# Performance work log

Hardware: AMD Instinct MI355X
Metric: run time of the kernel (lower is better)

Reference implementation:

```python
import jax, jax.numpy as jnp
import numpy as np

N = 50000
E = 1_600_000
IN_C = 128
HID = 64
HEADS = 2
OUT_C = 16
NEG_SLOPE = 0.2
EPS = 1e-16


def setup_inputs() -> dict:
    key = jax.random.key(0)
    ks = jax.random.split(key, 10)
    x = jax.random.normal(ks[0], (N, IN_C), dtype=jnp.float32)
    edge_index = jax.random.randint(ks[1], (2, E), 0, N, dtype=jnp.int64)
    # layer 1: in -> HEADS * HID, concat=True
    s1 = 1.0 / np.sqrt(IN_C)
    W1 = jax.random.normal(ks[2], (IN_C, HEADS * HID), dtype=jnp.float32) * s1
    att_src1 = jax.random.normal(ks[3], (HEADS, HID), dtype=jnp.float32) * (1.0 / np.sqrt(HID))
    att_dst1 = jax.random.normal(ks[4], (HEADS, HID), dtype=jnp.float32) * (1.0 / np.sqrt(HID))
    b1 = jnp.zeros((HEADS * HID,), dtype=jnp.float32)
    # layer 2: HEADS*HID -> OUT_C, heads=1
    s2 = 1.0 / np.sqrt(HEADS * HID)
    W2 = jax.random.normal(ks[5], (HEADS * HID, OUT_C), dtype=jnp.float32) * s2
    att_src2 = jax.random.normal(ks[6], (1, OUT_C), dtype=jnp.float32) * (1.0 / np.sqrt(OUT_C))
    att_dst2 = jax.random.normal(ks[7], (1, OUT_C), dtype=jnp.float32) * (1.0 / np.sqrt(OUT_C))
    b2 = jnp.zeros((OUT_C,), dtype=jnp.float32)
    return {"x": x, "W1": W1, "att_src1": att_src1, "att_dst1": att_dst1, "b1": b1,
            "W2": W2, "att_src2": att_src2, "att_dst2": att_dst2, "b2": b2,
            "edge_index": edge_index}


def gat_conv(x, edge_index, W, att_src, att_dst, bias, heads, out_ch):
    """PyG-style GATConv: per-head linear, additive attention, softmax over
    incoming edges of each destination node, scatter-add aggregation."""
    n = x.shape[0]
    src, dst = edge_index[0], edge_index[1]
    h = (x @ W).reshape(n, heads, out_ch)                # [N,H,C]
    a_src = jnp.einsum('nhc,hc->nh', h, att_src)          # [N,H]
    a_dst = jnp.einsum('nhc,hc->nh', h, att_dst)          # [N,H]
    e = a_src[src] + a_dst[dst]                           # [E,H]
    e = jnp.where(e >= 0, e, NEG_SLOPE * e)               # LeakyReLU(0.2)
    e_max = jax.ops.segment_max(e, dst, num_segments=n)   # [N,H]
    e_max = jax.lax.stop_gradient(jnp.where(jnp.isfinite(e_max), e_max, 0.0))
    e_exp = jnp.exp(e - e_max[dst])                       # [E,H]
    denom = jax.ops.segment_sum(e_exp, dst, num_segments=n)  # [N,H]
    alpha = e_exp / (denom[dst] + EPS)                    # [E,H]
    msg = h[src] * alpha[:, :, None]                      # [E,H,C] (dominant traffic)
    out = jax.ops.segment_sum(msg, dst, num_segments=n)   # [N,H,C]
    return out.reshape(n, heads * out_ch) + bias


def reference(x, W1, att_src1, att_dst1, b1, W2, att_src2, att_dst2, b2, edge_index):
    h = gat_conv(x, edge_index, W1, att_src1, att_dst1, b1, HEADS, HID)
    h = jax.nn.elu(h)
    h = gat_conv(h, edge_index, W2, att_src2, att_dst2, b2, 1, OUT_C)
    return jax.nn.softmax(h, axis=1)
```

## Files before the change

kernel.cpp:

```cpp
#include <hip/hip_runtime.h>
#include <hip/hip_fp16.h>
#include <cstdint>
#include <cstddef>

#define N_NODES 50000
#define N_EDGES 1600000
#define NEG_SLOPE 0.2f
#define GAT_EPS 1e-16f

#define NCHUNK 128
#define CE (N_EDGES / NCHUNK)
#define NBKT 196
#define GEMM_BLOCKS 782

typedef _Float16 half8v __attribute__((ext_vector_type(8)));
typedef _Float16 half4v __attribute__((ext_vector_type(4)));
typedef float f32x4 __attribute__((ext_vector_type(4)));



__global__ __launch_bounds__(256) void k_gh(
    const float* __restrict__ x, const float* __restrict__ W1,
    const float* __restrict__ W2, const float* __restrict__ b1,
    const float* __restrict__ att_src, const float* __restrict__ att_dst,
    _Float16* __restrict__ h1p, float* __restrict__ a_src, float* __restrict__ a_dst,
    const int* __restrict__ ei, int* __restrict__ coarse,
    float* __restrict__ w2tp, float* __restrict__ b1p) {
    __shared__ __align__(16) char smem[34816];
    int t = threadIdx.x;
    int b = blockIdx.x;
    if (b == GEMM_BLOCKS + NCHUNK) {
        for (int i = t; i < 2112; i += 256) {
            int j = i / 132, kp = i % 132;
            float v = 0.f;
            if (kp < 128) {
                int real = (kp & 7) * 16 + (kp >> 3);
                v = W2[real * 16 + j];
            }
            w2tp[i] = v;
        }
        if (t < 128) {
            int real = (t & 7) * 16 + (t >> 3);
            b1p[t] = b1[real];
        }
        return;
    }
    if (b >= GEMM_BLOCKS) {
        int* h = (int*)smem;
        int g = b - GEMM_BLOCKS;
        if (t < NBKT) h[t] = 0;
        __syncthreads();
        int e0 = g * CE;
        for (int e = e0 + t; e < e0 + CE; e += 256)
            atomicAdd(&h[ei[N_EDGES + e] >> 8], 1);
        __syncthreads();
        if (t < NBKT) coarse[t * NCHUNK + g] = h[t];
        return;
    }
    _Float16* wl = (_Float16*)smem;
    for (int j = t; j < 16384; j += 256) {
        int k = j >> 7, c = j & 127;
        wl[c * 136 + k] = (_Float16)W1[j];
    }
    __syncthreads();
    int wv = t >> 6, lane = t & 63;
    int m = lane & 15, q = lane >> 4;
    int nb = b * 64 + wv * 16;
    int grow = nb + m;
    const float* xrow = x + (size_t)((grow < N_NODES) ? grow : (N_NODES - 1)) * 128;
    f32x4 acc[8];
#pragma unroll
    for (int ct = 0; ct < 8; ++ct) acc[ct] = (f32x4){0.f, 0.f, 0.f, 0.f};
#pragma unroll
    for (int kc = 0; kc < 4; ++kc) {
        float4 u0 = *(const float4*)(xrow + kc * 32 + q * 8);
        float4 u1 = *(const float4*)(xrow + kc * 32 + q * 8 + 4);
        half8v a;
        a[0] = (_Float16)u0.x; a[1] = (_Float16)u0.y;
        a[2] = (_Float16)u0.z; a[3] = (_Float16)u0.w;
        a[4] = (_Float16)u1.x; a[5] = (_Float16)u1.y;
        a[6] = (_Float16)u1.z; a[7] = (_Float16)u1.w;
#pragma unroll
        for (int ct = 0; ct < 8; ++ct) {
            half8v bf = *(const half8v*)(wl + (ct * 16 + m) * 136 + kc * 32 + q * 8);
            acc[ct] = __builtin_amdgcn_mfma_f32_16x16x32_f16(a, bf, acc[ct], 0, 0, 0);
        }
    }
    float att_s[8], att_d[8];
#pragma unroll
    for (int ct = 0; ct < 8; ++ct) {
        att_s[ct] = att_src[ct * 16 + m];
        att_d[ct] = att_dst[ct * 16 + m];
    }
#pragma unroll
    for (int r = 0; r < 4; ++r) {
        int gn = nb + q * 4 + r;
        half8v hv;
        float ps0 = 0.f, ps1 = 0.f, pd0 = 0.f, pd1 = 0.f;
#pragma unroll
        for (int ct = 0; ct < 8; ++ct) {
            float v = acc[ct][r];
            hv[ct] = (_Float16)v;
            if (ct < 4) { ps0 += v * att_s[ct]; pd0 += v * att_d[ct]; }
            else        { ps1 += v * att_s[ct]; pd1 += v * att_d[ct]; }
        }
#pragma unroll
        for (int off = 8; off >= 1; off >>= 1) {
            ps0 += __shfl_xor(ps0, off, 64);
            ps1 += __shfl_xor(ps1, off, 64);
            pd0 += __shfl_xor(pd0, off, 64);
            pd1 += __shfl_xor(pd1, off, 64);
        }
        if (gn < N_NODES) {
            *(half8v*)(h1p + (size_t)gn * 128 + m * 8) = hv;
            if (m == 0) {
                a_src[gn * 2 + 0] = ps0;
                a_src[gn * 2 + 1] = ps1;
                a_dst[gn * 2 + 0] = pd0;
                a_dst[gn * 2 + 1] = pd1;
            }
        }
    }
}


__global__ __launch_bounds__(1024) void k_cscan(const int* __restrict__ coarse,
                                                int* __restrict__ cbase,
                                                int* __restrict__ bb,
                                                int* __restrict__ row_start) {
    __shared__ int cl[NBKT * NCHUNK];
    __shared__ int btot[NBKT];
    __shared__ int bbase[NBKT];
    int t = threadIdx.x;
    for (int i = t; i < NBKT * NCHUNK; i += 1024) cl[i] = coarse[i];
    __syncthreads();
    if (t < NBKT) {
        int s = 0;
        for (int g = 0; g < NCHUNK; ++g) s += cl[t * NCHUNK + g];
        btot[t] = s;
    }
    __syncthreads();
    if (t == 0) {
        int base = 0;
        for (int b = 0; b < NBKT; ++b) { bbase[b] = base; base += btot[b]; }
    }
    __syncthreads();
    if (t < NBKT) {
        int run = bbase[t];
        bb[t] = run;
        for (int g = 0; g < NCHUNK; ++g) {
            cbase[t * NCHUNK + g] = run;
            run += cl[t * NCHUNK + g];
        }
    }
    if (t == 0) { bb[NBKT] = N_EDGES; row_start[N_NODES] = N_EDGES; }
}

__global__ __launch_bounds__(256) void k_partition(const int* __restrict__ ei,
                                                   const int* __restrict__ cbase,
                                                   int2* __restrict__ part) {
    __shared__ int loc[NBKT];
    int t = threadIdx.x, g = blockIdx.x;
    if (t < NBKT) loc[t] = cbase[t * NCHUNK + g];
    __syncthreads();
    int e0 = g * CE;
    for (int e = e0 + t; e < e0 + CE; e += 256) {
        int s = ei[e], d = ei[N_EDGES + e];
        int slot = atomicAdd(&loc[d >> 8], 1);
        part[slot] = make_int2(s, d);
    }
}

__global__ __launch_bounds__(256) void k_local(const int2* __restrict__ part,
                                               const int* __restrict__ bb,
                                               const float* __restrict__ a_src1,
                                               const float* __restrict__ a_dst1,
                                               int* __restrict__ row_start,
                                               int4* __restrict__ csr,
                                               int* __restrict__ csrc) {
    __shared__ int hist[256];
    __shared__ int fillv[256];
    __shared__ float2 adl[256];
    __shared__ int wtot[4];
    int t = threadIdx.x, b = blockIdx.x;
    int n0 = b << 8;
    int es = bb[b], ee = bb[b + 1];
    hist[t] = 0;
    if (n0 + t < N_NODES) adl[t] = ((const float2*)a_dst1)[n0 + t];
    __syncthreads();
    for (int e = es + t; e < ee; e += 256) atomicAdd(&hist[part[e].y - n0], 1);
    __syncthreads();
    int lane = t & 63, w = t >> 6;
    int v = hist[t], x = v;
#pragma unroll
    for (int off = 1; off < 64; off <<= 1) {
        int y = __shfl_up(x, off, 64);
        if (lane >= off) x += y;
    }
    if (lane == 63) wtot[w] = x;
    __syncthreads();
    int woff = 0;
    for (int i = 0; i < w; ++i) woff += wtot[i];
    int excl = woff + x - v;
    if (n0 + t < N_NODES) row_start[n0 + t] = es + excl;
    fillv[t] = excl;
    __syncthreads();
    for (int e = es + t; e < ee; e += 256) {
        int2 sd = part[e];
        int j = sd.y - n0;
        int slot = es + atomicAdd(&fillv[j], 1);
        float2 as = ((const float2*)a_src1)[sd.x];
        float2 ad = adl[j];
        float e0 = as.x + ad.x; e0 = (e0 >= 0.f) ? e0 : NEG_SLOPE * e0;
        float e1 = as.y + ad.y; e1 = (e1 >= 0.f) ? e1 : NEG_SLOPE * e1;
        csr[slot] = make_int4(sd.x, __float_as_int(expf(e0)), __float_as_int(expf(e1)), 0);
        csrc[slot] = sd.x;
    }
}


__global__ __launch_bounds__(256) void k_agg1f(
    const int* __restrict__ row_start, const int4* __restrict__ csr,
    const _Float16* __restrict__ h1p, const float* __restrict__ b1p,
    const float* __restrict__ w2tp,
    const float* __restrict__ att_src2, const float* __restrict__ att_dst2,
    float* __restrict__ h2, float* __restrict__ as2, float* __restrict__ ad2) {
    __shared__ float w2l[16 * 132];
    __shared__ float rows[4][128];
    __shared__ int4 elds[4][64];
    int t = threadIdx.x;
    for (int i = t; i < 528; i += 256) ((float4*)w2l)[i] = ((const float4*)w2tp)[i];
    __syncthreads();
    int wv = t >> 6, lane = t & 63;
    int d = blockIdx.x * 4 + wv;
    int row = row_start[d], end = row_start[d + 1];
    int m16 = lane & 15;
    int qt = lane >> 4;
    uint32_t moff = (uint32_t)m16 * 16u;
    const char* hbase = (const char*)h1p;
    float den0 = 0.f, den1 = 0.f;
    float acc[8];
#pragma unroll
    for (int i = 0; i < 8; ++i) acc[i] = 0.f;
    for (int base = row; base < end; base += 64) {
        int m = end - base;
        if (m > 64) m = 64;
        int idx = base + lane;
        int idxc = (idx < end) ? idx : (end - 1);
        int4 e4 = csr[idxc];
        if (idx >= end) { e4.y = 0; e4.z = 0; }
        elds[wv][lane] = e4;
        int nc = (m + 3) >> 2;
        auto step = [&](int p) {
            int4 md = elds[wv][p * 4 + qt];
            float w0 = __int_as_float(md.y);
            float w1 = __int_as_float(md.z);
            uint32_t off = ((uint32_t)md.x << 8) + moff;
            half8v hv = *(const half8v*)(hbase + off);
            den0 += w0;
            den1 += w1;
            acc[0] += w0 * (float)hv[0];
            acc[1] += w0 * (float)hv[1];
            acc[2] += w0 * (float)hv[2];
            acc[3] += w0 * (float)hv[3];
            acc[4] += w1 * (float)hv[4];
            acc[5] += w1 * (float)hv[5];
            acc[6] += w1 * (float)hv[6];
            acc[7] += w1 * (float)hv[7];
        };
        int p = 0;
        for (; p + 4 <= nc; p += 4) {
            step(p); step(p + 1); step(p + 2); step(p + 3);
        }
        for (; p < nc; ++p) step(p);
    }
#pragma unroll
    for (int i = 0; i < 8; ++i) {
        acc[i] += __shfl_xor(acc[i], 16, 64);
        acc[i] += __shfl_xor(acc[i], 32, 64);
    }
    den0 += __shfl_xor(den0, 16, 64);
    den0 += __shfl_xor(den0, 32, 64);
    den1 += __shfl_xor(den1, 16, 64);
    den1 += __shfl_xor(den1, 32, 64);
    float inv0 = 1.f / (den0 + GAT_EPS);
    float inv1 = 1.f / (den1 + GAT_EPS);
    float4 blo = ((const float4*)b1p)[m16 * 2];
    float4 bhi = ((const float4*)b1p)[m16 * 2 + 1];
    float o[8];
    o[0] = acc[0] * inv0 + blo.x;
    o[1] = acc[1] * inv0 + blo.y;
    o[2] = acc[2] * inv0 + blo.z;
    o[3] = acc[3] * inv0 + blo.w;
    o[4] = acc[4] * inv1 + bhi.x;
    o[5] = acc[5] * inv1 + bhi.y;
    o[6] = acc[6] * inv1 + bhi.z;
    o[7] = acc[7] * inv1 + bhi.w;
#pragma unroll
    for (int i = 0; i < 8; ++i) o[i] = (o[i] > 0.f) ? o[i] : expm1f(o[i]);
    if (qt == 0) {
        *(float4*)(&rows[wv][m16 * 8]) = make_float4(o[0], o[1], o[2], o[3]);
        *(float4*)(&rows[wv][m16 * 8 + 4]) = make_float4(o[4], o[5], o[6], o[7]);
    }
    int j = lane & 15, q = lane >> 4;
    const float* r = rows[wv];
    const float* wt = &w2l[j * 132];
    int k0 = q * 32;
    float acc2 = 0.f;
#pragma unroll
    for (int sI = 0; sI < 8; ++sI) {
        int sp = ((sI + q) & 7) * 4;
        float4 rv = *(const float4*)(r + k0 + sp);
        float4 w4 = *(const float4*)(wt + k0 + sp);
        acc2 += rv.x * w4.x + rv.y * w4.y + rv.z * w4.z + rv.w * w4.w;
    }
    acc2 += __shfl_xor(acc2, 16, 64);
    acc2 += __shfl_xor(acc2, 32, 64);
    if (lane < 16) {
        h2[(size_t)d * 16 + j] = acc2;
        float ps = acc2 * att_src2[j];
        float pd = acc2 * att_dst2[j];
#pragma unroll
        for (int off = 8; off >= 1; off >>= 1) {
            ps += __shfl_xor(ps, off, 64);
            pd += __shfl_xor(pd, off, 64);
        }
        if (lane == 0) { as2[d] = ps; ad2[d] = pd; }
    }
}


__global__ __launch_bounds__(256) void k_agg2(
    const int* __restrict__ row_start, const int* __restrict__ csrc,
    const float* __restrict__ h2, const float* __restrict__ as2,
    const float* __restrict__ ad2, const float* __restrict__ b2,
    float* __restrict__ out) {
    __shared__ int2 elds[4][64];
    int t = threadIdx.x;
    int wv = t >> 6, lane = t & 63;
    int d = blockIdx.x * 4 + wv;
    int row = row_start[d], end = row_start[d + 1];
    float ad = ad2[d];
    int c = lane & 15, qt = lane >> 4;
    float den = 0.f, acc = 0.f;
    for (int base = row; base < end; base += 64) {
        int m = end - base;
        if (m > 64) m = 64;
        int idx = base + lane;
        int idxc = (idx < end) ? idx : (end - 1);
        int s = csrc[idxc];
        float w = 0.f;
        if (idx < end) {
            float e = as2[s] + ad;
            e = (e >= 0.f) ? e : NEG_SLOPE * e;
            w = expf(e);
        }
        den += w;
        elds[wv][lane] = make_int2(s, __float_as_int(w));
        int nc = (m + 3) >> 2;
        auto step = [&](int p) {
            int2 md = elds[wv][p * 4 + qt];
            float wj = __int_as_float(md.y);
            acc += wj * h2[(size_t)md.x * 16 + c];
        };
        int p = 0;
        for (; p + 4 <= nc; p += 4) {
            step(p); step(p + 1); step(p + 2); step(p + 3);
        }
        for (; p < nc; ++p) step(p);
    }
#pragma unroll
    for (int off = 32; off >= 1; off >>= 1) den += __shfl_xor(den, off, 64);
    acc += __shfl_xor(acc, 16, 64);
    acc += __shfl_xor(acc, 32, 64);
    float v = acc / (den + GAT_EPS) + b2[c];
    float mmax = v;
#pragma unroll
    for (int off = 8; off >= 1; off >>= 1) mmax = fmaxf(mmax, __shfl_xor(mmax, off, 16));
    float ex = expf(v - mmax);
    float sum = ex;
#pragma unroll
    for (int off = 8; off >= 1; off >>= 1) sum += __shfl_xor(sum, off, 16);
    if (lane < 16) out[(size_t)d * 16 + c] = ex / sum;
}


extern "C" void kernel_launch(void* const* d_in, const int* in_sizes, int n_in,
                              void* d_out, int out_size, void* d_ws, size_t ws_size,
                              hipStream_t stream) {
    const float* x        = (const float*)d_in[0];
    const float* W1       = (const float*)d_in[1];
    const float* att_src1 = (const float*)d_in[2];
    const float* att_dst1 = (const float*)d_in[3];
    const float* b1       = (const float*)d_in[4];
    const float* W2       = (const float*)d_in[5];
    const float* att_src2 = (const float*)d_in[6];
    const float* att_dst2 = (const float*)d_in[7];
    const float* b2       = (const float*)d_in[8];
    const int*   ei       = (const int*)d_in[9];

    char* p = (char*)d_ws;
    auto alloc = [&](size_t bytes) {
        char* r = p;
        p += (bytes + 255) & ~(size_t)255;
        return r;
    };
    _Float16* h1p  = (_Float16*)alloc(sizeof(_Float16) * (size_t)N_NODES * 128);
    float* w2tp    = (float*)alloc(sizeof(float) * 16 * 132);
    float* b1p     = (float*)alloc(sizeof(float) * 128);
    float* h2      = (float*)alloc(sizeof(float) * (size_t)N_NODES * 16);
    float* a_src   = (float*)alloc(sizeof(float) * N_NODES * 2);
    float* a_dst   = (float*)alloc(sizeof(float) * N_NODES * 2);
    float* as2     = (float*)alloc(sizeof(float) * N_NODES);
    float* ad2     = (float*)alloc(sizeof(float) * N_NODES);
    int* coarse    = (int*)alloc(sizeof(int) * NBKT * NCHUNK);
    int* cbase     = (int*)alloc(sizeof(int) * NBKT * NCHUNK);
    int* bb        = (int*)alloc(sizeof(int) * (NBKT + 1));
    int* row_start = (int*)alloc(sizeof(int) * (N_NODES + 1));
    int2* part     = (int2*)alloc(sizeof(int2) * (size_t)N_EDGES);
    int4* csr      = (int4*)alloc(sizeof(int4) * (size_t)N_EDGES);
    int* csrc      = (int*)alloc(sizeof(int) * (size_t)N_EDGES);

    k_gh<<<GEMM_BLOCKS + NCHUNK + 1, 256, 0, stream>>>(x, W1, W2, b1, att_src1, att_dst1,
                                                       h1p, a_src, a_dst, ei, coarse, w2tp, b1p);
    k_cscan<<<1, 1024, 0, stream>>>(coarse, cbase, bb, row_start);
    k_partition<<<NCHUNK, 256, 0, stream>>>(ei, cbase, part);
    k_local<<<NBKT, 256, 0, stream>>>(part, bb, a_src, a_dst, row_start, csr, csrc);
    k_agg1f<<<N_NODES / 4, 256, 0, stream>>>(row_start, csr, h1p, b1p, w2tp, att_src2, att_dst2, h2, as2, ad2);
    k_agg2<<<N_NODES / 4, 256, 0, stream>>>(row_start, csrc, h2, as2, ad2, b2, (float*)d_out);
}
```

Before: 264.4 us.

## Replace two-level bucketed CSR build with global histogram, scan, and atomic scatter

```diff
diff --git a/kernel.cpp b/kernel.cpp
--- a/kernel.cpp
+++ b/kernel.cpp
@@ -10,8 +10,8 @@
 
 #define NCHUNK 128
 #define CE (N_EDGES / NCHUNK)
-#define NBKT 196
 #define GEMM_BLOCKS 782
+#define SCAN_CHK 49
 
 typedef _Float16 half8v __attribute__((ext_vector_type(8)));
 typedef _Float16 half4v __attribute__((ext_vector_type(4)));
@@ -24,7 +24,7 @@
     const float* __restrict__ W2, const float* __restrict__ b1,
     const float* __restrict__ att_src, const float* __restrict__ att_dst,
     _Float16* __restrict__ h1p, float* __restrict__ a_src, float* __restrict__ a_dst,
-    const int* __restrict__ ei, int* __restrict__ coarse,
+    const int* __restrict__ ei, int* __restrict__ hist,
     float* __restrict__ w2tp, float* __restrict__ b1p) {
     __shared__ __align__(16) char smem[34816];
     int t = threadIdx.x;
@@ -46,15 +46,10 @@
         return;
     }
     if (b >= GEMM_BLOCKS) {
-        int* h = (int*)smem;
         int g = b - GEMM_BLOCKS;
-        if (t < NBKT) h[t] = 0;
-        __syncthreads();
         int e0 = g * CE;
         for (int e = e0 + t; e < e0 + CE; e += 256)
-            atomicAdd(&h[ei[N_EDGES + e] >> 8], 1);
-        __syncthreads();
-        if (t < NBKT) coarse[t * NCHUNK + g] = h[t];
+            atomicAdd(&hist[ei[N_EDGES + e]], 1);
         return;
     }
     _Float16* wl = (_Float16*)smem;
@@ -124,97 +119,53 @@
 }
 
 
-__global__ __launch_bounds__(1024) void k_cscan(const int* __restrict__ coarse,
-                                                int* __restrict__ cbase,
-                                                int* __restrict__ bb,
-                                                int* __restrict__ row_start) {
-    __shared__ int cl[NBKT * NCHUNK];
-    __shared__ int btot[NBKT];
-    __shared__ int bbase[NBKT];
+__global__ __launch_bounds__(1024) void k_scan(const int* __restrict__ hist,
+                                               int* __restrict__ row_start,
+                                               int* __restrict__ fill) {
+    __shared__ int wt[16];
     int t = threadIdx.x;
-    for (int i = t; i < NBKT * NCHUNK; i += 1024) cl[i] = coarse[i];
-    __syncthreads();
-    if (t < NBKT) {
-        int s = 0;
-        for (int g = 0; g < NCHUNK; ++g) s += cl[t * NCHUNK + g];
-        btot[t] = s;
-    }
-    __syncthreads();
-    if (t == 0) {
-        int base = 0;
-        for (int b = 0; b < NBKT; ++b) { bbase[b] = base; base += btot[b]; }
-    }
-    __syncthreads();
-    if (t < NBKT) {
-        int run = bbase[t];
-        bb[t] = run;
-        for (int g = 0; g < NCHUNK; ++g) {
-            cbase[t * NCHUNK + g] = run;
-            run += cl[t * NCHUNK + g];
-        }
-    }
-    if (t == 0) { bb[NBKT] = N_EDGES; row_start[N_NODES] = N_EDGES; }
-}
-
-__global__ __launch_bounds__(256) void k_partition(const int* __restrict__ ei,
-                                                   const int* __restrict__ cbase,
-                                                   int2* __restrict__ part) {
-    __shared__ int loc[NBKT];
-    int t = threadIdx.x, g = blockIdx.x;
-    if (t < NBKT) loc[t] = cbase[t * NCHUNK + g];
-    __syncthreads();
-    int e0 = g * CE;
-    for (int e = e0 + t; e < e0 + CE; e += 256) {
-        int s = ei[e], d = ei[N_EDGES + e];
-        int slot = atomicAdd(&loc[d >> 8], 1);
-        part[slot] = make_int2(s, d);
-    }
-}
-
-__global__ __launch_bounds__(256) void k_local(const int2* __restrict__ part,
-                                               const int* __restrict__ bb,
-                                               const float* __restrict__ a_src1,
-                                               const float* __restrict__ a_dst1,
-                                               int* __restrict__ row_start,
-                                               int4* __restrict__ csr,
-                                               int* __restrict__ csrc) {
-    __shared__ int hist[256];
-    __shared__ int fillv[256];
-    __shared__ float2 adl[256];
-    __shared__ int wtot[4];
-    int t = threadIdx.x, b = blockIdx.x;
-    int n0 = b << 8;
-    int es = bb[b], ee = bb[b + 1];
-    hist[t] = 0;
-    if (n0 + t < N_NODES) adl[t] = ((const float2*)a_dst1)[n0 + t];
-    __syncthreads();
-    for (int e = es + t; e < ee; e += 256) atomicAdd(&hist[part[e].y - n0], 1);
-    __syncthreads();
+    int lo = t * SCAN_CHK;
+    int hi = lo + SCAN_CHK;
+    if (lo > N_NODES) lo = N_NODES;
+    if (hi > N_NODES) hi = N_NODES;
+    int s = 0;
+    for (int i = lo; i < hi; ++i) s += hist[i];
     int lane = t & 63, w = t >> 6;
-    int v = hist[t], x = v;
+    int x = s;
 #pragma unroll
     for (int off = 1; off < 64; off <<= 1) {
         int y = __shfl_up(x, off, 64);
         if (lane >= off) x += y;
     }
-    if (lane == 63) wtot[w] = x;
+    if (lane == 63) wt[w] = x;
     __syncthreads();
     int woff = 0;
-    for (int i = 0; i < w; ++i) woff += wtot[i];
-    int excl = woff + x - v;
-    if (n0 + t < N_NODES) row_start[n0 + t] = es + excl;
-    fillv[t] = excl;
-    __syncthreads();
-    for (int e = es + t; e < ee; e += 256) {
-        int2 sd = part[e];
-        int j = sd.y - n0;
-        int slot = es + atomicAdd(&fillv[j], 1);
-        float2 as = ((const float2*)a_src1)[sd.x];
-        float2 ad = adl[j];
+    for (int i = 0; i < w; ++i) woff += wt[i];
+    int run = woff + x - s;
+    for (int i = lo; i < hi; ++i) {
+        row_start[i] = run;
+        fill[i] = run;
+        run += hist[i];
+    }
+    if (t == 1023) row_start[N_NODES] = N_EDGES;
+}
+
+
+__global__ __launch_bounds__(256) void k_scatter(
+    const int* __restrict__ ei, const float* __restrict__ a_src1,
+    const float* __restrict__ a_dst1, int* __restrict__ fill,
+    int4* __restrict__ csr, int* __restrict__ csrc) {
+    int tid = blockIdx.x * 256 + threadIdx.x;
+    int stride = gridDim.x * 256;
+    for (int e = tid; e < N_EDGES; e += stride) {
+        int s = ei[e], d = ei[N_EDGES + e];
+        float2 as = ((const float2*)a_src1)[s];
+        float2 ad = ((const float2*)a_dst1)[d];
         float e0 = as.x + ad.x; e0 = (e0 >= 0.f) ? e0 : NEG_SLOPE * e0;
         float e1 = as.y + ad.y; e1 = (e1 >= 0.f) ? e1 : NEG_SLOPE * e1;
-        csr[slot] = make_int4(sd.x, __float_as_int(expf(e0)), __float_as_int(expf(e1)), 0);
-        csrc[slot] = sd.x;
+        int slot = atomicAdd(&fill[d], 1);
+        csr[slot] = make_int4(s, __float_as_int(expf(e0)), __float_as_int(expf(e1)), 0);
+        csrc[slot] = s;
     }
 }
 
@@ -413,19 +364,17 @@
     float* a_dst   = (float*)alloc(sizeof(float) * N_NODES * 2);
     float* as2     = (float*)alloc(sizeof(float) * N_NODES);
     float* ad2     = (float*)alloc(sizeof(float) * N_NODES);
-    int* coarse    = (int*)alloc(sizeof(int) * NBKT * NCHUNK);
-    int* cbase     = (int*)alloc(sizeof(int) * NBKT * NCHUNK);
-    int* bb        = (int*)alloc(sizeof(int) * (NBKT + 1));
+    int* hist      = (int*)alloc(sizeof(int) * (N_NODES + 1));
+    int* fill      = (int*)alloc(sizeof(int) * N_NODES);
     int* row_start = (int*)alloc(sizeof(int) * (N_NODES + 1));
-    int2* part     = (int2*)alloc(sizeof(int2) * (size_t)N_EDGES);
     int4* csr      = (int4*)alloc(sizeof(int4) * (size_t)N_EDGES);
     int* csrc      = (int*)alloc(sizeof(int) * (size_t)N_EDGES);
 
+    hipMemsetAsync(hist, 0, sizeof(int) * N_NODES, stream);
     k_gh<<<GEMM_BLOCKS + NCHUNK + 1, 256, 0, stream>>>(x, W1, W2, b1, att_src1, att_dst1,
-                                                       h1p, a_src, a_dst, ei, coarse, w2tp, b1p);
-    k_cscan<<<1, 1024, 0, stream>>>(coarse, cbase, bb, row_start);
-    k_partition<<<NCHUNK, 256, 0, stream>>>(ei, cbase, part);
-    k_local<<<NBKT, 256, 0, stream>>>(part, bb, a_src, a_dst, row_start, csr, csrc);
+                                                       h1p, a_src, a_dst, ei, hist, w2tp, b1p);
+    k_scan<<<1, 1024, 0, stream>>>(hist, row_start, fill);
+    k_scatter<<<2048, 256, 0, stream>>>(ei, a_src, a_dst, fill, csr, csrc);
     k_agg1f<<<N_NODES / 4, 256, 0, stream>>>(row_start, csr, h1p, b1p, w2tp, att_src2, att_dst2, h2, as2, ad2);
     k_agg2<<<N_NODES / 4, 256, 0, stream>>>(row_start, csrc, h2, as2, ad2, b2, (float*)d_out);
 }
```

Result: slower. 445.5 us (+68.5%).

## Pack partition edges to 32 bits, split CSR record, parallelize bucket scan

Applied to the files above, without the earlier changes.

```diff
diff --git a/kernel.cpp b/kernel.cpp
--- a/kernel.cpp
+++ b/kernel.cpp
@@ -129,20 +129,31 @@
                                                 int* __restrict__ bb,
                                                 int* __restrict__ row_start) {
     __shared__ int cl[NBKT * NCHUNK];
-    __shared__ int btot[NBKT];
+    __shared__ int btot[256];
     __shared__ int bbase[NBKT];
+    __shared__ int wt4[4];
     int t = threadIdx.x;
     for (int i = t; i < NBKT * NCHUNK; i += 1024) cl[i] = coarse[i];
     __syncthreads();
-    if (t < NBKT) {
+    if (t < 256) {
         int s = 0;
-        for (int g = 0; g < NCHUNK; ++g) s += cl[t * NCHUNK + g];
+        if (t < NBKT)
+            for (int g = 0; g < NCHUNK; ++g) s += cl[t * NCHUNK + g];
         btot[t] = s;
-    }
-    __syncthreads();
-    if (t == 0) {
-        int base = 0;
-        for (int b = 0; b < NBKT; ++b) { bbase[b] = base; base += btot[b]; }
+        int lane = t & 63, w = t >> 6;
+        int x = s;
+#pragma unroll
+        for (int off = 1; off < 64; off <<= 1) {
+            int y = __shfl_up(x, off, 64);
+            if (lane >= off) x += y;
+        }
+        if (lane == 63) wt4[w] = x;
+        __syncthreads();
+        int woff = 0;
+        for (int i = 0; i < w; ++i) woff += wt4[i];
+        if (t < NBKT) bbase[t] = woff + x - s;
+    } else {
+        __syncthreads();
     }
     __syncthreads();
     if (t < NBKT) {
@@ -158,7 +169,7 @@
 
 __global__ __launch_bounds__(256) void k_partition(const int* __restrict__ ei,
                                                    const int* __restrict__ cbase,
-                                                   int2* __restrict__ part) {
+                                                   unsigned int* __restrict__ part) {
     __shared__ int loc[NBKT];
     int t = threadIdx.x, g = blockIdx.x;
     if (t < NBKT) loc[t] = cbase[t * NCHUNK + g];
@@ -167,17 +178,17 @@
     for (int e = e0 + t; e < e0 + CE; e += 256) {
         int s = ei[e], d = ei[N_EDGES + e];
         int slot = atomicAdd(&loc[d >> 8], 1);
-        part[slot] = make_int2(s, d);
-    }
-}
-
-__global__ __launch_bounds__(256) void k_local(const int2* __restrict__ part,
+        part[slot] = ((unsigned int)d << 16) | (unsigned int)s;
+    }
+}
+
+__global__ __launch_bounds__(256) void k_local(const unsigned int* __restrict__ part,
                                                const int* __restrict__ bb,
                                                const float* __restrict__ a_src1,
                                                const float* __restrict__ a_dst1,
                                                int* __restrict__ row_start,
-                                               int4* __restrict__ csr,
-                                               int* __restrict__ csrc) {
+                                               int* __restrict__ csrc,
+                                               float2* __restrict__ cw) {
     __shared__ int hist[256];
     __shared__ int fillv[256];
     __shared__ float2 adl[256];
@@ -188,7 +199,7 @@
     hist[t] = 0;
     if (n0 + t < N_NODES) adl[t] = ((const float2*)a_dst1)[n0 + t];
     __syncthreads();
-    for (int e = es + t; e < ee; e += 256) atomicAdd(&hist[part[e].y - n0], 1);
+    for (int e = es + t; e < ee; e += 256) atomicAdd(&hist[(part[e] >> 16) - n0], 1);
     __syncthreads();
     int lane = t & 63, w = t >> 6;
     int v = hist[t], x = v;
@@ -206,21 +217,23 @@
     fillv[t] = excl;
     __syncthreads();
     for (int e = es + t; e < ee; e += 256) {
-        int2 sd = part[e];
-        int j = sd.y - n0;
+        unsigned int sd = part[e];
+        int s = (int)(sd & 0xFFFFu);
+        int j = (int)(sd >> 16) - n0;
         int slot = es + atomicAdd(&fillv[j], 1);
-        float2 as = ((const float2*)a_src1)[sd.x];
+        float2 as = ((const float2*)a_src1)[s];
         float2 ad = adl[j];
         float e0 = as.x + ad.x; e0 = (e0 >= 0.f) ? e0 : NEG_SLOPE * e0;
         float e1 = as.y + ad.y; e1 = (e1 >= 0.f) ? e1 : NEG_SLOPE * e1;
-        csr[slot] = make_int4(sd.x, __float_as_int(expf(e0)), __float_as_int(expf(e1)), 0);
-        csrc[slot] = sd.x;
+        csrc[slot] = s;
+        cw[slot] = make_float2(expf(e0), expf(e1));
     }
 }
 
 
 __global__ __launch_bounds__(256) void k_agg1f(
-    const int* __restrict__ row_start, const int4* __restrict__ csr,
+    const int* __restrict__ row_start, const int* __restrict__ csrc,
+    const float2* __restrict__ cw,
     const _Float16* __restrict__ h1p, const float* __restrict__ b1p,
     const float* __restrict__ w2tp,
     const float* __restrict__ att_src2, const float* __restrict__ att_dst2,
@@ -247,9 +260,10 @@
         if (m > 64) m = 64;
         int idx = base + lane;
         int idxc = (idx < end) ? idx : (end - 1);
-        int4 e4 = csr[idxc];
-        if (idx >= end) { e4.y = 0; e4.z = 0; }
-        elds[wv][lane] = e4;
+        int s = csrc[idxc];
+        float2 wv2 = cw[idxc];
+        if (idx >= end) { wv2.x = 0.f; wv2.y = 0.f; }
+        elds[wv][lane] = make_int4(s, __float_as_int(wv2.x), __float_as_int(wv2.y), 0);
         int nc = (m + 3) >> 2;
         auto step = [&](int p) {
             int4 md = elds[wv][p * 4 + qt];
@@ -417,15 +431,15 @@
     int* cbase     = (int*)alloc(sizeof(int) * NBKT * NCHUNK);
     int* bb        = (int*)alloc(sizeof(int) * (NBKT + 1));
     int* row_start = (int*)alloc(sizeof(int) * (N_NODES + 1));
-    int2* part     = (int2*)alloc(sizeof(int2) * (size_t)N_EDGES);
-    int4* csr      = (int4*)alloc(sizeof(int4) * (size_t)N_EDGES);
+    unsigned int* part = (unsigned int*)alloc(sizeof(unsigned int) * (size_t)N_EDGES);
     int* csrc      = (int*)alloc(sizeof(int) * (size_t)N_EDGES);
+    float2* cw     = (float2*)alloc(sizeof(float2) * (size_t)N_EDGES);
 
     k_gh<<<GEMM_BLOCKS + NCHUNK + 1, 256, 0, stream>>>(x, W1, W2, b1, att_src1, att_dst1,
                                                        h1p, a_src, a_dst, ei, coarse, w2tp, b1p);
     k_cscan<<<1, 1024, 0, stream>>>(coarse, cbase, bb, row_start);
     k_partition<<<NCHUNK, 256, 0, stream>>>(ei, cbase, part);
-    k_local<<<NBKT, 256, 0, stream>>>(part, bb, a_src, a_dst, row_start, csr, csrc);
-    k_agg1f<<<N_NODES / 4, 256, 0, stream>>>(row_start, csr, h1p, b1p, w2tp, att_src2, att_dst2, h2, as2, ad2);
+    k_local<<<NBKT, 256, 0, stream>>>(part, bb, a_src, a_dst, row_start, csrc, cw);
+    k_agg1f<<<N_NODES / 4, 256, 0, stream>>>(row_start, csrc, cw, h1p, b1p, w2tp, att_src2, att_dst2, h2, as2, ad2);
     k_agg2<<<N_NODES / 4, 256, 0, stream>>>(row_start, csrc, h2, as2, ad2, b2, (float*)d_out);
 }
```

After: 258.7 us. 1.02x faster.
